# Optimization experiments

Measured on AMD Instinct MI355X. Metric: run time of the kernel, lower is better.

## Reference

```python
import jax, jax.numpy as jnp
import numpy as np

NUM_USERS = 200_000
NUM_ITEMS = 100_000
N = NUM_USERS + NUM_ITEMS
D = 32
E = 9_600_000
N_LAYERS = 3


def setup_inputs() -> dict:
    key = jax.random.key(0)
    k1, k2, k3, k4, k5 = jax.random.split(key, 5)
    rows = jax.random.randint(k1, (E,), 0, N, dtype=jnp.int32)
    cols = jax.random.randint(k2, (E,), 0, N, dtype=jnp.int32)
    # normalized-adjacency-like positive values
    vals = jax.random.uniform(k3, (E,), dtype=jnp.float32) * 0.05
    # xavier-uniform-ish embedding init
    bound = float(np.sqrt(6.0 / (NUM_USERS + D)))
    user_w = jax.random.uniform(k4, (NUM_USERS, D), dtype=jnp.float32,
                                minval=-bound, maxval=bound)
    bound_i = float(np.sqrt(6.0 / (NUM_ITEMS + D)))
    item_w = jax.random.uniform(k5, (NUM_ITEMS, D), dtype=jnp.float32,
                                minval=-bound_i, maxval=bound_i)
    return {"rows": rows, "cols": cols, "vals": vals,
            "user_w": user_w, "item_w": item_w}


def _spmm(rows, cols, vals, x):
    # A_hat @ x for COO A_hat: gather source features, scale, scatter-add to rows.
    msgs = vals[:, None] * x[cols]                 # [E, D]
    return jax.ops.segment_sum(msgs, rows, num_segments=N)  # [N, D]


def reference(rows, cols, vals, user_w, item_w):
    x0 = jnp.concatenate([user_w, item_w], axis=0)  # [N, D]
    x = x0
    acc = x0
    for _ in range(N_LAYERS):
        x = _spmm(rows, cols, vals, x)
        acc = acc + x
    x_mean = acc / (N_LAYERS + 1)                   # mean over layer stack
    users = x_mean[:NUM_USERS]
    items = x_mean[NUM_USERS:]
    return (users, items)
```

## Files before the change

kernel.cpp:

```cpp
#include <hip/hip_runtime.h>

#define NUM_USERS 200000
#define NUM_ITEMS 100000
#define NN (NUM_USERS + NUM_ITEMS)
#define D 32
#define NE 9600000
#define TOTAL (NN * D)

#define RPB2 128
#define B2 ((NN + RPB2 - 1) / RPB2)
#define CAP 5120

#define TPB_A 1024
#define EPT 16
#define EPB_A (TPB_A * EPT)

#define TPB_H 1024
#define EPT_H 32
#define EPB_H (TPB_H * EPT_H)
#define NB_H ((NE + EPB_H - 1) / EPB_H)

__global__ __launch_bounds__(256) void init_x_acc(
    const float4* __restrict__ user_w, const float4* __restrict__ item_w,
    float4* __restrict__ x, float4* __restrict__ acc) {
    int i = blockIdx.x * 256 + threadIdx.x;
    const int total4 = TOTAL / 4;
    const int ub4 = (NUM_USERS * D) / 4;
    if (i < total4) {
        float4 v = (i < ub4) ? user_w[i] : item_w[i - ub4];
        x[i] = v;
        acc[i] = v;
    }
}

__global__ __launch_bounds__(TPB_H) void bucket_hist(
    const int4* __restrict__ rows4, int* __restrict__ bcounts) {
    __shared__ int hist[B2];
    int tid = threadIdx.x;
    for (int i = tid; i < B2; i += TPB_H) hist[i] = 0;
    __syncthreads();
    int base4 = blockIdx.x * (EPB_H / 4);
    #pragma unroll
    for (int k = 0; k < EPT_H / 4; ++k) {
        int i4 = base4 + k * TPB_H + tid;
        if (i4 < NE / 4) {
            int4 r = rows4[i4];
            atomicAdd(&hist[r.x >> 7], 1);
            atomicAdd(&hist[r.y >> 7], 1);
            atomicAdd(&hist[r.z >> 7], 1);
            atomicAdd(&hist[r.w >> 7], 1);
        }
    }
    __syncthreads();
    for (int b = tid; b < B2; b += TPB_H) {
        int c = hist[b];
        if (c) atomicAdd(&bcounts[b], c);
    }
}

__global__ __launch_bounds__(1024) void scan_buckets(
    const int* __restrict__ bcounts, int* __restrict__ bstart,
    int* __restrict__ bfill) {
    __shared__ int lds[1024];
    int t = threadIdx.x;
    int v[4];
    int s = 0;
    #pragma unroll
    for (int k = 0; k < 4; ++k) {
        int b = t * 4 + k;
        v[k] = (b < B2) ? bcounts[b] : 0;
        s += v[k];
    }
    lds[t] = s;
    __syncthreads();
    for (int off = 1; off < 1024; off <<= 1) {
        int u = (t >= off) ? lds[t - off] : 0;
        __syncthreads();
        lds[t] += u;
        __syncthreads();
    }
    int ex = lds[t] - s;
    #pragma unroll
    for (int k = 0; k < 4; ++k) {
        int b = t * 4 + k;
        if (b < B2) { bstart[b] = ex; bfill[b] = ex; }
        ex += v[k];
    }
    if (t == 1023) bstart[B2] = ex;
}

__global__ __launch_bounds__(TPB_A) void partition_edges(
    const int4* __restrict__ rows4, const int4* __restrict__ cols4,
    const float4* __restrict__ vals4, int* __restrict__ bfill,
    int2* __restrict__ temp) {
    __shared__ int hist[B2];
    int tid = threadIdx.x;
    for (int i = tid; i < B2; i += TPB_A) hist[i] = 0;
    __syncthreads();

    int base4 = blockIdx.x * (EPB_A / 4);
    int brank[EPT];

    #pragma unroll
    for (int k = 0; k < EPT / 4; ++k) {
        int i4 = base4 + k * TPB_A + tid;
        if (i4 < NE / 4) {
            int4 r = rows4[i4];
            int b0 = r.x >> 7, b1 = r.y >> 7, b2 = r.z >> 7, b3 = r.w >> 7;
            brank[k * 4 + 0] = (b0 << 16) | atomicAdd(&hist[b0], 1);
            brank[k * 4 + 1] = (b1 << 16) | atomicAdd(&hist[b1], 1);
            brank[k * 4 + 2] = (b2 << 16) | atomicAdd(&hist[b2], 1);
            brank[k * 4 + 3] = (b3 << 16) | atomicAdd(&hist[b3], 1);
        }
    }
    __syncthreads();
    for (int b = tid; b < B2; b += TPB_A) {
        int c = hist[b];
        if (c) hist[b] = atomicAdd(&bfill[b], c);
    }
    __syncthreads();

    #pragma unroll
    for (int k = 0; k < EPT / 4; ++k) {
        int i4 = base4 + k * TPB_A + tid;
        if (i4 < NE / 4) {
            int4 r = rows4[i4];
            int4 c = cols4[i4];
            float4 v = vals4[i4];
            int br, pos; int2 cv;
            br = brank[k * 4 + 0]; pos = hist[br >> 16] + (br & 0xFFFF);
            cv.x = ((r.x & 127) << 19) | c.x; cv.y = __float_as_int(v.x); temp[pos] = cv;
            br = brank[k * 4 + 1]; pos = hist[br >> 16] + (br & 0xFFFF);
            cv.x = ((r.y & 127) << 19) | c.y; cv.y = __float_as_int(v.y); temp[pos] = cv;
            br = brank[k * 4 + 2]; pos = hist[br >> 16] + (br & 0xFFFF);
            cv.x = ((r.z & 127) << 19) | c.z; cv.y = __float_as_int(v.z); temp[pos] = cv;
            br = brank[k * 4 + 3]; pos = hist[br >> 16] + (br & 0xFFFF);
            cv.x = ((r.w & 127) << 19) | c.w; cv.y = __float_as_int(v.w); temp[pos] = cv;
        }
    }
}

__global__ __launch_bounds__(256) void sort_bucket2(
    const int* __restrict__ bstart, const int2* __restrict__ temp,
    int* __restrict__ row_start, int2* __restrict__ colval) {
    __shared__ int2 stage[CAP];
    __shared__ int lstart[RPB2];
    __shared__ int lfill[RPB2];
    int b = blockIdx.x;
    int row0 = b * RPB2;
    int rcount = NN - row0; if (rcount > RPB2) rcount = RPB2;
    int tid = threadIdx.x;
    int s = bstart[b];
    int count = bstart[b + 1] - s;

    if (tid < RPB2) lfill[tid] = 0;
    __syncthreads();

    for (int i = tid; i < count; i += 256) {
        int rl = temp[s + i].x >> 19;
        atomicAdd(&lfill[rl], 1);
    }
    __syncthreads();

    int val = (tid < RPB2) ? lfill[tid] : 0;
    if (tid < RPB2) lstart[tid] = val;
    __syncthreads();
    for (int off = 1; off < RPB2; off <<= 1) {
        int u = (tid >= off && tid < RPB2) ? lstart[tid - off] : 0;
        __syncthreads();
        if (tid < RPB2) lstart[tid] += u;
        __syncthreads();
    }
    int ex = (tid < RPB2) ? lstart[tid] - val : 0;
    if (tid < RPB2) {
        lstart[tid] = ex;
        lfill[tid] = 0;
        if (tid < rcount) row_start[row0 + tid] = s + ex;
    }
    if (b == 0 && tid == 0) row_start[NN] = NE;
    __syncthreads();

    if (count <= CAP) {
        for (int i = tid; i < count; i += 256) {
            int2 e = temp[s + i];
            int rl = e.x >> 19;
            int pos = lstart[rl] + atomicAdd(&lfill[rl], 1);
            stage[pos] = make_int2(e.x & 0x7FFFF, e.y);
        }
        __syncthreads();
        for (int i = tid; i < count; i += 256) colval[s + i] = stage[i];
    } else {
        for (int i = tid; i < count; i += 256) {
            int2 e = temp[s + i];
            int rl = e.x >> 19;
            int pos = lstart[rl] + atomicAdd(&lfill[rl], 1);
            colval[s + pos] = make_int2(e.x & 0x7FFFF, e.y);
        }
    }
}

template <bool LAST>
__global__ __launch_bounds__(256) void spmm_csr(
    const int* __restrict__ row_start, const int2* __restrict__ colval,
    const float* __restrict__ x, float* __restrict__ y,
    float* __restrict__ acc) {
    int lane = threadIdx.x & 31;
    int row = blockIdx.x * 8 + (threadIdx.x >> 5);
    if (row >= NN) return;
    int s = row_start[row];
    int e = row_start[row + 1];
    float s0 = 0.f, s1 = 0.f, s2 = 0.f, s3 = 0.f;
    float s4 = 0.f, s5 = 0.f, s6 = 0.f, s7 = 0.f;
    int i = s;
    for (; i + 7 < e; i += 8) {
        int2 a0 = colval[i];
        int2 a1 = colval[i + 1];
        int2 a2 = colval[i + 2];
        int2 a3 = colval[i + 3];
        int2 a4 = colval[i + 4];
        int2 a5 = colval[i + 5];
        int2 a6 = colval[i + 6];
        int2 a7 = colval[i + 7];
        s0 += __int_as_float(a0.y) * x[a0.x * D + lane];
        s1 += __int_as_float(a1.y) * x[a1.x * D + lane];
        s2 += __int_as_float(a2.y) * x[a2.x * D + lane];
        s3 += __int_as_float(a3.y) * x[a3.x * D + lane];
        s4 += __int_as_float(a4.y) * x[a4.x * D + lane];
        s5 += __int_as_float(a5.y) * x[a5.x * D + lane];
        s6 += __int_as_float(a6.y) * x[a6.x * D + lane];
        s7 += __int_as_float(a7.y) * x[a7.x * D + lane];
    }
    for (; i < e; ++i) {
        int2 a = colval[i];
        s0 += __int_as_float(a.y) * x[a.x * D + lane];
    }
    float sum = ((s0 + s1) + (s2 + s3)) + ((s4 + s5) + (s6 + s7));
    int idx = row * D + lane;
    y[idx] = sum;
    float a = acc[idx] + sum;
    acc[idx] = LAST ? a * 0.25f : a;
}

extern "C" void kernel_launch(void* const* d_in, const int* in_sizes, int n_in,
                              void* d_out, int out_size, void* d_ws, size_t ws_size,
                              hipStream_t stream) {
    const int*   rows   = (const int*)d_in[0];
    const int*   cols   = (const int*)d_in[1];
    const float* vals   = (const float*)d_in[2];
    const float* user_w = (const float*)d_in[3];
    const float* item_w = (const float*)d_in[4];

    float* acc = (float*)d_out;

    float* x = (float*)d_ws;
    float* y = x + (size_t)TOTAL;
    int2*  temp = (int2*)d_ws;
    int2*  colval = (int2*)(y + (size_t)TOTAL);
    int*   bcounts = (int*)(colval + (size_t)NE);
    int*   bstart = bcounts + B2;
    int*   bfill = bstart + (B2 + 1);
    int*   row_start = bfill + B2;

    const int vec_blocks   = (TOTAL / 4 + 255) / 256;
    const int partA_blocks = (NE + EPB_A - 1) / EPB_A;
    const int row_blocks   = (NN + 7) / 8;

    hipMemsetAsync(bcounts, 0, (size_t)B2 * sizeof(int), stream);
    bucket_hist<<<NB_H, TPB_H, 0, stream>>>((const int4*)rows, bcounts);
    scan_buckets<<<1, 1024, 0, stream>>>(bcounts, bstart, bfill);
    partition_edges<<<partA_blocks, TPB_A, 0, stream>>>(
        (const int4*)rows, (const int4*)cols, (const float4*)vals, bfill, temp);
    sort_bucket2<<<B2, 256, 0, stream>>>(bstart, temp, row_start, colval);

    init_x_acc<<<vec_blocks, 256, 0, stream>>>(
        (const float4*)user_w, (const float4*)item_w, (float4*)x, (float4*)acc);

    spmm_csr<false><<<row_blocks, 256, 0, stream>>>(row_start, colval, x, y, acc);
    spmm_csr<false><<<row_blocks, 256, 0, stream>>>(row_start, colval, y, x, acc);
    spmm_csr<true ><<<row_blocks, 256, 0, stream>>>(row_start, colval, x, y, acc);
}
```

Baseline: 969.5 us.

## Store layer embeddings in fp16 for SpMM gathers and avoid re-reading rows

New measurement: 932.2 us. 3.8% less time.

```diff
diff --git a/kernel.cpp b/kernel.cpp
--- a/kernel.cpp
+++ b/kernel.cpp
@@ -1,4 +1,6 @@
 #include <hip/hip_runtime.h>
+#include <hip/hip_fp16.h>
+#include <stdint.h>
 
 #define NUM_USERS 200000
 #define NUM_ITEMS 100000
@@ -22,14 +24,19 @@
 
 __global__ __launch_bounds__(256) void init_x_acc(
     const float4* __restrict__ user_w, const float4* __restrict__ item_w,
-    float4* __restrict__ x, float4* __restrict__ acc) {
+    ushort4* __restrict__ xh, float4* __restrict__ acc) {
     int i = blockIdx.x * 256 + threadIdx.x;
     const int total4 = TOTAL / 4;
     const int ub4 = (NUM_USERS * D) / 4;
     if (i < total4) {
         float4 v = (i < ub4) ? user_w[i] : item_w[i - ub4];
-        x[i] = v;
         acc[i] = v;
+        ushort4 h;
+        h.x = __half_as_ushort(__float2half(v.x));
+        h.y = __half_as_ushort(__float2half(v.y));
+        h.z = __half_as_ushort(__float2half(v.z));
+        h.w = __half_as_ushort(__float2half(v.w));
+        xh[i] = h;
     }
 }
 
@@ -99,18 +106,19 @@
     __syncthreads();
 
     int base4 = blockIdx.x * (EPB_A / 4);
-    int brank[EPT];
+    uint32_t brank[EPT];
 
     #pragma unroll
     for (int k = 0; k < EPT / 4; ++k) {
         int i4 = base4 + k * TPB_A + tid;
         if (i4 < NE / 4) {
             int4 r = rows4[i4];
-            int b0 = r.x >> 7, b1 = r.y >> 7, b2 = r.z >> 7, b3 = r.w >> 7;
-            brank[k * 4 + 0] = (b0 << 16) | atomicAdd(&hist[b0], 1);
-            brank[k * 4 + 1] = (b1 << 16) | atomicAdd(&hist[b1], 1);
-            brank[k * 4 + 2] = (b2 << 16) | atomicAdd(&hist[b2], 1);
-            brank[k * 4 + 3] = (b3 << 16) | atomicAdd(&hist[b3], 1);
+            uint32_t b0 = (uint32_t)r.x >> 7, b1 = (uint32_t)r.y >> 7;
+            uint32_t b2 = (uint32_t)r.z >> 7, b3 = (uint32_t)r.w >> 7;
+            brank[k * 4 + 0] = (b0 << 20) | (uint32_t)((r.x & 127) << 13) | (uint32_t)atomicAdd(&hist[b0], 1);
+            brank[k * 4 + 1] = (b1 << 20) | (uint32_t)((r.y & 127) << 13) | (uint32_t)atomicAdd(&hist[b1], 1);
+            brank[k * 4 + 2] = (b2 << 20) | (uint32_t)((r.z & 127) << 13) | (uint32_t)atomicAdd(&hist[b2], 1);
+            brank[k * 4 + 3] = (b3 << 20) | (uint32_t)((r.w & 127) << 13) | (uint32_t)atomicAdd(&hist[b3], 1);
         }
     }
     __syncthreads();
@@ -124,18 +132,17 @@
     for (int k = 0; k < EPT / 4; ++k) {
         int i4 = base4 + k * TPB_A + tid;
         if (i4 < NE / 4) {
-            int4 r = rows4[i4];
             int4 c = cols4[i4];
             float4 v = vals4[i4];
-            int br, pos; int2 cv;
-            br = brank[k * 4 + 0]; pos = hist[br >> 16] + (br & 0xFFFF);
-            cv.x = ((r.x & 127) << 19) | c.x; cv.y = __float_as_int(v.x); temp[pos] = cv;
-            br = brank[k * 4 + 1]; pos = hist[br >> 16] + (br & 0xFFFF);
-            cv.x = ((r.y & 127) << 19) | c.y; cv.y = __float_as_int(v.y); temp[pos] = cv;
-            br = brank[k * 4 + 2]; pos = hist[br >> 16] + (br & 0xFFFF);
-            cv.x = ((r.z & 127) << 19) | c.z; cv.y = __float_as_int(v.z); temp[pos] = cv;
-            br = brank[k * 4 + 3]; pos = hist[br >> 16] + (br & 0xFFFF);
-            cv.x = ((r.w & 127) << 19) | c.w; cv.y = __float_as_int(v.w); temp[pos] = cv;
+            uint32_t br; int pos; int2 cv;
+            br = brank[k * 4 + 0]; pos = hist[br >> 20] + (int)(br & 0x1FFFu);
+            cv.x = (int)(((br >> 13) & 127u) << 19) | c.x; cv.y = __float_as_int(v.x); temp[pos] = cv;
+            br = brank[k * 4 + 1]; pos = hist[br >> 20] + (int)(br & 0x1FFFu);
+            cv.x = (int)(((br >> 13) & 127u) << 19) | c.y; cv.y = __float_as_int(v.y); temp[pos] = cv;
+            br = brank[k * 4 + 2]; pos = hist[br >> 20] + (int)(br & 0x1FFFu);
+            cv.x = (int)(((br >> 13) & 127u) << 19) | c.z; cv.y = __float_as_int(v.z); temp[pos] = cv;
+            br = brank[k * 4 + 3]; pos = hist[br >> 20] + (int)(br & 0x1FFFu);
+            cv.x = (int)(((br >> 13) & 127u) << 19) | c.w; cv.y = __float_as_int(v.w); temp[pos] = cv;
         }
     }
 }
@@ -202,7 +209,7 @@
 template <bool LAST>
 __global__ __launch_bounds__(256) void spmm_csr(
     const int* __restrict__ row_start, const int2* __restrict__ colval,
-    const float* __restrict__ x, float* __restrict__ y,
+    const __half* __restrict__ xh, __half* __restrict__ yh,
     float* __restrict__ acc) {
     int lane = threadIdx.x & 31;
     int row = blockIdx.x * 8 + (threadIdx.x >> 5);
@@ -221,22 +228,22 @@
         int2 a5 = colval[i + 5];
         int2 a6 = colval[i + 6];
         int2 a7 = colval[i + 7];
-        s0 += __int_as_float(a0.y) * x[a0.x * D + lane];
-        s1 += __int_as_float(a1.y) * x[a1.x * D + lane];
-        s2 += __int_as_float(a2.y) * x[a2.x * D + lane];
-        s3 += __int_as_float(a3.y) * x[a3.x * D + lane];
-        s4 += __int_as_float(a4.y) * x[a4.x * D + lane];
-        s5 += __int_as_float(a5.y) * x[a5.x * D + lane];
-        s6 += __int_as_float(a6.y) * x[a6.x * D + lane];
-        s7 += __int_as_float(a7.y) * x[a7.x * D + lane];
+        s0 += __int_as_float(a0.y) * __half2float(xh[a0.x * D + lane]);
+        s1 += __int_as_float(a1.y) * __half2float(xh[a1.x * D + lane]);
+        s2 += __int_as_float(a2.y) * __half2float(xh[a2.x * D + lane]);
+        s3 += __int_as_float(a3.y) * __half2float(xh[a3.x * D + lane]);
+        s4 += __int_as_float(a4.y) * __half2float(xh[a4.x * D + lane]);
+        s5 += __int_as_float(a5.y) * __half2float(xh[a5.x * D + lane]);
+        s6 += __int_as_float(a6.y) * __half2float(xh[a6.x * D + lane]);
+        s7 += __int_as_float(a7.y) * __half2float(xh[a7.x * D + lane]);
     }
     for (; i < e; ++i) {
         int2 a = colval[i];
-        s0 += __int_as_float(a.y) * x[a.x * D + lane];
+        s0 += __int_as_float(a.y) * __half2float(xh[a.x * D + lane]);
     }
     float sum = ((s0 + s1) + (s2 + s3)) + ((s4 + s5) + (s6 + s7));
     int idx = row * D + lane;
-    y[idx] = sum;
+    if (!LAST) yh[idx] = __float2half(sum);
     float a = acc[idx] + sum;
     acc[idx] = LAST ? a * 0.25f : a;
 }
@@ -252,10 +259,10 @@
 
     float* acc = (float*)d_out;
 
-    float* x = (float*)d_ws;
-    float* y = x + (size_t)TOTAL;
+    __half* xh = (__half*)d_ws;
+    __half* yh = xh + (size_t)TOTAL;
     int2*  temp = (int2*)d_ws;
-    int2*  colval = (int2*)(y + (size_t)TOTAL);
+    int2*  colval = (int2*)((char*)d_ws + 2ull * (size_t)TOTAL * sizeof(float));
     int*   bcounts = (int*)(colval + (size_t)NE);
     int*   bstart = bcounts + B2;
     int*   bfill = bstart + (B2 + 1);
@@ -273,9 +280,9 @@
     sort_bucket2<<<B2, 256, 0, stream>>>(bstart, temp, row_start, colval);
 
     init_x_acc<<<vec_blocks, 256, 0, stream>>>(
-        (const float4*)user_w, (const float4*)item_w, (float4*)x, (float4*)acc);
-
-    spmm_csr<false><<<row_blocks, 256, 0, stream>>>(row_start, colval, x, y, acc);
-    spmm_csr<false><<<row_blocks, 256, 0, stream>>>(row_start, colval, y, x, acc);
-    spmm_csr<true ><<<row_blocks, 256, 0, stream>>>(row_start, colval, x, y, acc);
-}
+        (const float4*)user_w, (const float4*)item_w, (ushort4*)xh, (float4*)acc);
+
+    spmm_csr<false><<<row_blocks, 256, 0, stream>>>(row_start, colval, xh, yh, acc);
+    spmm_csr<false><<<row_blocks, 256, 0, stream>>>(row_start, colval, yh, xh, acc);
+    spmm_csr<true ><<<row_blocks, 256, 0, stream>>>(row_start, colval, xh, yh, acc);
+}
```
